# Kernel tuning notes

Measured on AMD Instinct MI355X. Metric: run time of the kernel, lower is better.

Reference implementation:

```python
import jax, jax.numpy as jnp
import numpy as np


def setup_inputs() -> dict:
    key = jax.random.key(0)
    ks = jax.random.split(key, 8)
    b, s1, s2 = 16, 512, 40
    video_dim, text_dim, attn_dim = 1024, 300, 256
    return {
        "video": jax.random.normal(ks[0], (b, s1, video_dim), dtype=jnp.float32),
        "text": jax.random.normal(ks[1], (b, s2, text_dim), dtype=jnp.float32),
        "w1": jax.random.normal(ks[2], (video_dim, attn_dim), dtype=jnp.float32),
        "w2": jax.random.normal(ks[3], (text_dim, attn_dim), dtype=jnp.float32),
        "w3": jax.random.normal(ks[4], (attn_dim, 1), dtype=jnp.float32),
        "bias": jax.random.normal(ks[5], (attn_dim,), dtype=jnp.float32),
        "w4": jax.random.normal(ks[6], (4 * attn_dim, 500), dtype=jnp.float32),
        "b4": jax.random.normal(ks[7], (500,), dtype=jnp.float32),
    }


def reference(video, text, w1, w2, w3, bias, w4, b4):
    # video: (b, s1, d1), text: (b, s2, d2)
    e = jnp.einsum("bsd,da->bsa", video, w1)   # (b, s1, a) -- also 'hh' in original
    f = jnp.einsum("btd,da->bta", text, w2)    # (b, s2, a)
    # additive attention energies: tanh over (b, s1, s2, a) broadcast sum
    h = jnp.tanh(e[:, :, None, :] + f[:, None, :, :] + bias)  # (b, s1, s2, a)
    logits = jnp.squeeze(jnp.einsum("bsta,ao->bsto", h, w3), -1)  # (b, s1, s2)
    # original expands logits over attn_dim then softmaxes dim=2; identical to
    # softmax over s2 of the scalar scores, broadcast afterwards.
    attn = jax.nn.softmax(logits, axis=2)  # (b, s1, s2)
    text_attn = jnp.einsum("bst,bta->bsa", attn, f)  # (b, s1, a)
    cont = jnp.concatenate(
        [e, text_attn, e * text_attn, e - text_attn], axis=-1
    )  # (b, s1, 4a)
    return jnp.tanh(cont) @ w4 + b4  # (b, s1, 500)
```

## Files before the change

kernel.cpp:

```cpp
#include <hip/hip_runtime.h>
#include <hip/hip_bf16.h>
#include <cstdint>

typedef __attribute__((ext_vector_type(8))) short bf16x8;
typedef __attribute__((ext_vector_type(4))) short bf16x4;
typedef __attribute__((ext_vector_type(4))) float f32x4;

#define TANH_SCALE 2.8853900817779268f
#define TANH_UNSCALE 0.34657359027997264f

__device__ __forceinline__ short cvt_bf16(float f) {
  union { float f; uint32_t u; } x; x.f = f;
  uint32_t r = x.u + 0x7FFFu + ((x.u >> 16) & 1u);
  return (short)(r >> 16);
}
__device__ __forceinline__ float bf16_to_f(short s) {
  union { uint32_t u; float f; } x; x.u = ((uint32_t)(uint16_t)s) << 16;
  return x.f;
}

__device__ __forceinline__ float tanh_fast(float x) {
  float e = __builtin_amdgcn_exp2f(x * TANH_SCALE);
  return 1.0f - 2.0f * __builtin_amdgcn_rcpf(e + 1.0f);
}
__device__ __forceinline__ float tanh_pre(float xs) {
  float e = __builtin_amdgcn_exp2f(xs);
  return 1.0f - 2.0f * __builtin_amdgcn_rcpf(e + 1.0f);
}

__global__ __launch_bounds__(256) void k_prep(const float* __restrict__ video,
                                              const float* __restrict__ text,
                                              const float* __restrict__ w1,
                                              const float* __restrict__ w2,
                                              const float* __restrict__ w4,
                                              short* __restrict__ vhi,
                                              short* __restrict__ vlo,
                                              short* __restrict__ w1h,
                                              short* __restrict__ w1l,
                                              short* __restrict__ w4T,
                                              short* __restrict__ th,
                                              short* __restrict__ tl,
                                              short* __restrict__ w2h,
                                              short* __restrict__ w2l) {
  __shared__ float tile[32][33];
  int bid = blockIdx.x;
  if (bid < 1024) {
    int i = bid * 256 + threadIdx.x;
    for (; i < 2097152; i += 1024 * 256) {
      float4 v = ((const float4*)video)[i];
      bf16x4 h, l;
      h.x = cvt_bf16(v.x); h.y = cvt_bf16(v.y); h.z = cvt_bf16(v.z); h.w = cvt_bf16(v.w);
      l.x = cvt_bf16(v.x - bf16_to_f(h.x));
      l.y = cvt_bf16(v.y - bf16_to_f(h.y));
      l.z = cvt_bf16(v.z - bf16_to_f(h.z));
      l.w = cvt_bf16(v.w - bf16_to_f(h.w));
      ((bf16x4*)vhi)[i] = h;
      ((bf16x4*)vlo)[i] = l;
    }
  } else if (bid < 1280) {
    int idx = bid - 1024;
    int r0 = (idx & 31) * 32, c0 = (idx >> 5) * 32;
    int j = threadIdx.x & 31, i0 = threadIdx.x >> 5;
    #pragma unroll
    for (int i = i0; i < 32; i += 8) tile[i][j] = w1[(size_t)(r0 + i) * 256 + c0 + j];
    __syncthreads();
    #pragma unroll
    for (int i = i0; i < 32; i += 8) {
      float v = tile[j][i];
      short h = cvt_bf16(v);
      w1h[(size_t)(c0 + i) * 1024 + r0 + j] = h;
      w1l[(size_t)(c0 + i) * 1024 + r0 + j] = cvt_bf16(v - bf16_to_f(h));
    }
  } else if (bid < 1792) {
    int idx = bid - 1280;
    int r0 = (idx & 31) * 32, c0 = (idx >> 5) * 32;
    int j = threadIdx.x & 31, i0 = threadIdx.x >> 5;
    #pragma unroll
    for (int i = i0; i < 32; i += 8) {
      int c = c0 + j;
      tile[i][j] = (c < 500) ? w4[(size_t)(r0 + i) * 500 + c] : 0.f;
    }
    __syncthreads();
    #pragma unroll
    for (int i = i0; i < 32; i += 8)
      w4T[(size_t)(c0 + i) * 1024 + r0 + j] = cvt_bf16(tile[j][i]);
  } else if (bid < 1952) {
    int idx = bid - 1792;
    int row = idx * 4 + (threadIdx.x >> 6);
    int cl = threadIdx.x & 63;
    const float* trow = text + (size_t)row * 300;
    short* hrow = th + (size_t)row * 320;
    short* lrow = tl + (size_t)row * 320;
    #pragma unroll
    for (int c0 = 0; c0 < 320; c0 += 64) {
      int c = c0 + cl;
      float v = (c < 300) ? trow[c] : 0.f;
      short h = cvt_bf16(v);
      hrow[c] = h;
      lrow[c] = cvt_bf16(v - bf16_to_f(h));
    }
  } else {
    int idx = bid - 1952;
    int rt = idx % 10, ct = idx / 10;
    int r0 = rt * 32, c0 = ct * 32;
    int j = threadIdx.x & 31, i0 = threadIdx.x >> 5;
    #pragma unroll
    for (int i = i0; i < 32; i += 8) {
      int r = r0 + i;
      tile[i][j] = (r < 300) ? w2[(size_t)r * 256 + c0 + j] : 0.f;
    }
    __syncthreads();
    #pragma unroll
    for (int i = i0; i < 32; i += 8) {
      float v = tile[j][i];
      short h = cvt_bf16(v);
      w2h[(size_t)(c0 + i) * 320 + r0 + j] = h;
      w2l[(size_t)(c0 + i) * 320 + r0 + j] = cvt_bf16(v - bf16_to_f(h));
    }
  }
}

__global__ __launch_bounds__(256) void k_gemm_split(const short* __restrict__ Ah,
                                                    const short* __restrict__ Al,
                                                    const short* __restrict__ BTh,
                                                    const short* __restrict__ BTl,
                                                    float* __restrict__ C,
                                                    int K, int ldc) {
  __shared__ __align__(16) short Ash[64][72];
  __shared__ __align__(16) short Asl[64][72];
  __shared__ __align__(16) short Bsh[64][72];
  __shared__ __align__(16) short Bsl[64][72];
  int m0 = blockIdx.x * 64, n0 = blockIdx.y * 64;
  int tid = threadIdx.x, lane = tid & 63, wave = tid >> 6;
  int wm = (wave & 1) * 32, wn = (wave >> 1) * 32;
  int srow = tid >> 3, sseg = (tid & 7) * 8;
  f32x4 acc[2][2];
  #pragma unroll
  for (int i = 0; i < 2; i++)
    #pragma unroll
    for (int j = 0; j < 2; j++) acc[i][j] = (f32x4){0.f, 0.f, 0.f, 0.f};
  int mrow = lane & 15, quad = lane >> 4;

  for (int k0 = 0; k0 < K; k0 += 64) {
    size_t aoff0 = (size_t)(m0 + srow) * K + k0 + sseg;
    size_t aoff1 = aoff0 + (size_t)32 * K;
    size_t boff0 = (size_t)(n0 + srow) * K + k0 + sseg;
    size_t boff1 = boff0 + (size_t)32 * K;
    bf16x8 a0h = *(const bf16x8*)(Ah + aoff0);
    bf16x8 a1h = *(const bf16x8*)(Ah + aoff1);
    bf16x8 a0l = *(const bf16x8*)(Al + aoff0);
    bf16x8 a1l = *(const bf16x8*)(Al + aoff1);
    bf16x8 b0h = *(const bf16x8*)(BTh + boff0);
    bf16x8 b1h = *(const bf16x8*)(BTh + boff1);
    bf16x8 b0l = *(const bf16x8*)(BTl + boff0);
    bf16x8 b1l = *(const bf16x8*)(BTl + boff1);
    __syncthreads();
    *(bf16x8*)&Ash[srow][sseg] = a0h;  *(bf16x8*)&Ash[srow + 32][sseg] = a1h;
    *(bf16x8*)&Asl[srow][sseg] = a0l;  *(bf16x8*)&Asl[srow + 32][sseg] = a1l;
    *(bf16x8*)&Bsh[srow][sseg] = b0h;  *(bf16x8*)&Bsh[srow + 32][sseg] = b1h;
    *(bf16x8*)&Bsl[srow][sseg] = b0l;  *(bf16x8*)&Bsl[srow + 32][sseg] = b1l;
    __syncthreads();
    #pragma unroll
    for (int ks = 0; ks < 2; ks++) {
      int kk = ks * 32 + quad * 8;
      bf16x8 ah[2], al[2], bh[2], bl[2];
      ah[0] = *(const bf16x8*)&Ash[wm + mrow][kk];
      ah[1] = *(const bf16x8*)&Ash[wm + 16 + mrow][kk];
      al[0] = *(const bf16x8*)&Asl[wm + mrow][kk];
      al[1] = *(const bf16x8*)&Asl[wm + 16 + mrow][kk];
      bh[0] = *(const bf16x8*)&Bsh[wn + mrow][kk];
      bh[1] = *(const bf16x8*)&Bsh[wn + 16 + mrow][kk];
      bl[0] = *(const bf16x8*)&Bsl[wn + mrow][kk];
      bl[1] = *(const bf16x8*)&Bsl[wn + 16 + mrow][kk];
      #pragma unroll
      for (int i = 0; i < 2; i++)
        #pragma unroll
        for (int j = 0; j < 2; j++) {
          acc[i][j] = __builtin_amdgcn_mfma_f32_16x16x32_bf16(ah[i], bh[j], acc[i][j], 0, 0, 0);
          acc[i][j] = __builtin_amdgcn_mfma_f32_16x16x32_bf16(ah[i], bl[j], acc[i][j], 0, 0, 0);
          acc[i][j] = __builtin_amdgcn_mfma_f32_16x16x32_bf16(al[i], bh[j], acc[i][j], 0, 0, 0);
        }
    }
  }
  int rbase = quad * 4;
  #pragma unroll
  for (int i = 0; i < 2; i++)
    #pragma unroll
    for (int j = 0; j < 2; j++) {
      int col = n0 + wn + j * 16 + mrow;
      #pragma unroll
      for (int r = 0; r < 4; r++) {
        int row = m0 + wm + i * 16 + rbase + r;
        C[(size_t)row * ldc + col] = acc[i][j][r];
      }
    }
}

__device__ __forceinline__ void load_lds16(void* lds, const void* g) {
  __builtin_amdgcn_global_load_lds(
      (const __attribute__((address_space(1))) void*)g,
      (__attribute__((address_space(3))) void*)lds, 16, 0, 0);
}

__global__ __launch_bounds__(256) void k_gemm_f(const short* __restrict__ A,
                                                const short* __restrict__ BT,
                                                const float* __restrict__ bias,
                                                float* __restrict__ C,
                                                int K, int ldc, int nstore) {
  __shared__ __align__(16) short As[128][64];
  __shared__ __align__(16) short Bs[64][64];
  int m0 = blockIdx.x * 128, n0 = blockIdx.y * 64;
  int tid = threadIdx.x, lane = tid & 63, wave = tid >> 6;
  int wm = wave * 32;
  int mrow = lane & 15, quad = lane >> 4;
  int lrow = lane >> 3, lseg = (lane & 7) * 8;

  f32x4 acc[2][4];
  #pragma unroll
  for (int i = 0; i < 2; i++)
    #pragma unroll
    for (int j = 0; j < 4; j++) acc[i][j] = (f32x4){0.f, 0.f, 0.f, 0.f};

  for (int k0 = 0; k0 < K; k0 += 64) {
    __syncthreads();
    #pragma unroll
    for (int i = 0; i < 4; i++) {
      int c = wave * 4 + i;
      load_lds16(&As[c * 8][0], A + (size_t)(m0 + c * 8 + lrow) * K + k0 + lseg);
    }
    #pragma unroll
    for (int i = 0; i < 2; i++) {
      int c = wave * 2 + i;
      load_lds16(&Bs[c * 8][0], BT + (size_t)(n0 + c * 8 + lrow) * K + k0 + lseg);
    }
    __syncthreads();
    #pragma unroll
    for (int ks = 0; ks < 2; ks++) {
      int kk = ks * 32 + quad * 8;
      bf16x8 af[2], bf[4];
      #pragma unroll
      for (int i = 0; i < 2; i++) af[i] = *(const bf16x8*)&As[wm + i * 16 + mrow][kk];
      #pragma unroll
      for (int j = 0; j < 4; j++) bf[j] = *(const bf16x8*)&Bs[j * 16 + mrow][kk];
      #pragma unroll
      for (int i = 0; i < 2; i++)
        #pragma unroll
        for (int j = 0; j < 4; j++)
          acc[i][j] = __builtin_amdgcn_mfma_f32_16x16x32_bf16(af[i], bf[j], acc[i][j], 0, 0, 0);
    }
  }
  int rbase = quad * 4;
  #pragma unroll
  for (int i = 0; i < 2; i++)
    #pragma unroll
    for (int j = 0; j < 4; j++) {
      int col = n0 + j * 16 + mrow;
      if (col < nstore) {
        float bv = bias[col];
        #pragma unroll
        for (int r = 0; r < 4; r++) {
          int row = m0 + wm + i * 16 + rbase + r;
          C[(size_t)row * ldc + col] = acc[i][j][r] + bv;
        }
      }
    }
}

__global__ __launch_bounds__(512) void k_middle(const float* __restrict__ e,
                                                const float* __restrict__ fb,
                                                const float* __restrict__ w3,
                                                const float* __restrict__ bias,
                                                short* __restrict__ cont) {
  __shared__ __align__(16) float fbs[40 * 256];
  __shared__ float lg[16][40];
  __shared__ float attn[16][40];
  int tid = threadIdx.x, wave = tid >> 6, lane = tid & 63;
  int la = lane & 31, half = lane >> 5;
  int row0 = blockIdx.x * 16;
  int b = row0 >> 9;
  int lgrow = wave + (half ? 8 : 0);
  int myrow = row0 + lgrow;

  const float4* fsrc = (const float4*)(fb + (size_t)b * 40 * 256);
  const float4* bias4 = (const float4*)bias;
  for (int i = tid; i < 40 * 64; i += 512) {
    float4 v = fsrc[i];
    float4 bb = bias4[i & 63];
    v.x = (v.x + bb.x) * TANH_SCALE; v.y = (v.y + bb.y) * TANH_SCALE;
    v.z = (v.z + bb.z) * TANH_SCALE; v.w = (v.w + bb.w) * TANH_SCALE;
    ((float4*)fbs)[i] = v;
  }
  __syncthreads();

  int a0 = la * 8;
  const float* erow = e + (size_t)myrow * 256 + a0;
  float4 e0 = *(const float4*)erow;
  float4 e1 = *(const float4*)(erow + 4);
  float4 w30 = *(const float4*)(w3 + a0);
  float4 w31 = *(const float4*)(w3 + a0 + 4);
  float4 bv0 = *(const float4*)(bias + a0);
  float4 bv1 = *(const float4*)(bias + a0 + 4);
  float4 es0, es1;
  es0.x = e0.x * TANH_SCALE; es0.y = e0.y * TANH_SCALE;
  es0.z = e0.z * TANH_SCALE; es0.w = e0.w * TANH_SCALE;
  es1.x = e1.x * TANH_SCALE; es1.y = e1.y * TANH_SCALE;
  es1.z = e1.z * TANH_SCALE; es1.w = e1.w * TANH_SCALE;

  for (int tc = 0; tc < 40; tc += 4) {
    float p[4];
    #pragma unroll
    for (int u = 0; u < 4; u++) {
      const float* fr = &fbs[(tc + u) * 256 + a0];
      float4 f0 = *(const float4*)fr;
      float4 f1 = *(const float4*)(fr + 4);
      p[u] = tanh_pre(es0.x + f0.x) * w30.x + tanh_pre(es0.y + f0.y) * w30.y
           + tanh_pre(es0.z + f0.z) * w30.z + tanh_pre(es0.w + f0.w) * w30.w
           + tanh_pre(es1.x + f1.x) * w31.x + tanh_pre(es1.y + f1.y) * w31.y
           + tanh_pre(es1.z + f1.z) * w31.z + tanh_pre(es1.w + f1.w) * w31.w;
    }
    #pragma unroll
    for (int s = 16; s >= 1; s >>= 1) {
      #pragma unroll
      for (int u = 0; u < 4; u++) p[u] += __shfl_xor(p[u], s, 64);
    }
    if (la == 0) {
      #pragma unroll
      for (int u = 0; u < 4; u++) lg[lgrow][tc + u] = p[u];
    }
  }

  auto softmax_row = [&](int r) {
    float x = (lane < 40) ? lg[r][lane] : -3.0e38f;
    float m = x;
    #pragma unroll
    for (int s = 32; s >= 1; s >>= 1) m = fmaxf(m, __shfl_xor(m, s, 64));
    float ex = (lane < 40) ? __builtin_amdgcn_exp2f((x - m) * 1.4426950408889634f) : 0.f;
    float ssum = ex;
    #pragma unroll
    for (int s = 32; s >= 1; s >>= 1) ssum += __shfl_xor(ssum, s, 64);
    if (lane < 40) attn[r][lane] = ex * __builtin_amdgcn_rcpf(ssum);
  };
  softmax_row(wave);
  softmax_row(wave + 8);

  float ac[8] = {0.f,0.f,0.f,0.f,0.f,0.f,0.f,0.f};
  for (int t = 0; t < 40; t++) {
    float w = attn[lgrow][t];
    const float* fr = &fbs[t * 256 + a0];
    float4 f0 = *(const float4*)fr;
    float4 f1 = *(const float4*)(fr + 4);
    ac[0] += w * f0.x; ac[1] += w * f0.y; ac[2] += w * f0.z; ac[3] += w * f0.w;
    ac[4] += w * f1.x; ac[5] += w * f1.y; ac[6] += w * f1.z; ac[7] += w * f1.w;
  }
  float tx[8];
  tx[0] = ac[0] * TANH_UNSCALE - bv0.x; tx[1] = ac[1] * TANH_UNSCALE - bv0.y;
  tx[2] = ac[2] * TANH_UNSCALE - bv0.z; tx[3] = ac[3] * TANH_UNSCALE - bv0.w;
  tx[4] = ac[4] * TANH_UNSCALE - bv1.x; tx[5] = ac[5] * TANH_UNSCALE - bv1.y;
  tx[6] = ac[6] * TANH_UNSCALE - bv1.z; tx[7] = ac[7] * TANH_UNSCALE - bv1.w;
  float ev[8] = {e0.x, e0.y, e0.z, e0.w, e1.x, e1.y, e1.z, e1.w};

  short* crow = cont + (size_t)myrow * 1024 + a0;
  auto st8 = [&](int off, const float* v) {
    bf16x8 pk;
    #pragma unroll
    for (int i = 0; i < 8; i++) pk[i] = cvt_bf16(v[i]);
    *(bf16x8*)(crow + off) = pk;
  };
  float s0[8], s1[8], s2[8], s3[8];
  #pragma unroll
  for (int i = 0; i < 8; i++) {
    s0[i] = tanh_fast(ev[i]);
    s1[i] = tanh_fast(tx[i]);
    s2[i] = tanh_fast(ev[i] * tx[i]);
    s3[i] = tanh_fast(ev[i] - tx[i]);
  }
  st8(0, s0); st8(256, s1); st8(512, s2); st8(768, s3);
}

extern "C" void kernel_launch(void* const* d_in, const int* in_sizes, int n_in,
                              void* d_out, int out_size, void* d_ws, size_t ws_size,
                              hipStream_t stream) {
  const float* video = (const float*)d_in[0];
  const float* text  = (const float*)d_in[1];
  const float* w1    = (const float*)d_in[2];
  const float* w2    = (const float*)d_in[3];
  const float* w3    = (const float*)d_in[4];
  const float* bias  = (const float*)d_in[5];
  const float* w4    = (const float*)d_in[6];
  const float* b4    = (const float*)d_in[7];
  float* out = (float*)d_out;
  char* ws = (char*)d_ws;

  short* video_hi = (short*)(ws);
  short* video_lo = (short*)(ws + 16777216);
  short* contbuf  = (short*)(ws + 16777216);
  short* w1T_hi   = (short*)(ws + 33554432);
  short* w1T_lo   = (short*)(ws + 34078720);
  short* w4T      = (short*)(ws + 34603008);
  float* fbuf     = (float*)(ws + 35651584);
  float* ebuf     = (float*)(ws + 36306944);
  short* text_hi  = (short*)(ws + 36306944);
  short* text_lo  = (short*)(ws + 36306944 + 409600);
  short* w2T_hi   = (short*)(ws + 36306944 + 819200);
  short* w2T_lo   = (short*)(ws + 36306944 + 1024000);

  k_prep<<<2032, 256, 0, stream>>>(video, text, w1, w2, w4,
                                   video_hi, video_lo, w1T_hi, w1T_lo, w4T,
                                   text_hi, text_lo, w2T_hi, w2T_lo);
  k_gemm_split<<<dim3(10, 4), 256, 0, stream>>>(text_hi, text_lo, w2T_hi, w2T_lo,
                                                fbuf, 320, 256);
  k_gemm_split<<<dim3(128, 4), 256, 0, stream>>>(video_hi, video_lo, w1T_hi, w1T_lo,
                                                 ebuf, 1024, 256);
  k_middle<<<512, 512, 0, stream>>>(ebuf, fbuf, w3, bias, contbuf);
  k_gemm_f<<<dim3(64, 8), 256, 0, stream>>>(contbuf, w4T, b4, out, 1024, 500, 500);
}
```

Measured before the change: 177.5 us.

## Split-K the video projection GEMM with larger M tiles, summing partials in middle kernel

```diff
diff --git a/kernel.cpp b/kernel.cpp
--- a/kernel.cpp
+++ b/kernel.cpp
@@ -202,6 +202,85 @@
       (__attribute__((address_space(3))) void*)lds, 16, 0, 0);
 }
 
+__global__ __launch_bounds__(256) void k_gemm_e2(const short* __restrict__ Ah,
+                                                 const short* __restrict__ Al,
+                                                 const short* __restrict__ BTh,
+                                                 const short* __restrict__ BTl,
+                                                 float* __restrict__ Cparts,
+                                                 int K, int ldc) {
+  __shared__ __align__(16) short Ash[128][64];
+  __shared__ __align__(16) short Asl[128][64];
+  __shared__ __align__(16) short Bsh[64][64];
+  __shared__ __align__(16) short Bsl[64][64];
+  int m0 = blockIdx.x * 128, n0 = blockIdx.y * 64;
+  int kz0 = blockIdx.z * 512;
+  int tid = threadIdx.x, lane = tid & 63, wave = tid >> 6;
+  int wm = wave * 32;
+  int mrow = lane & 15, quad = lane >> 4;
+  int lrow = lane >> 3, lseg = (lane & 7) * 8;
+
+  f32x4 acc[2][4];
+  #pragma unroll
+  for (int i = 0; i < 2; i++)
+    #pragma unroll
+    for (int j = 0; j < 4; j++) acc[i][j] = (f32x4){0.f, 0.f, 0.f, 0.f};
+
+  for (int k0 = kz0; k0 < kz0 + 512; k0 += 64) {
+    __syncthreads();
+    #pragma unroll
+    for (int i = 0; i < 4; i++) {
+      int c = wave * 4 + i;
+      size_t go = (size_t)(m0 + c * 8 + lrow) * K + k0 + lseg;
+      load_lds16(&Ash[c * 8][0], Ah + go);
+      load_lds16(&Asl[c * 8][0], Al + go);
+    }
+    #pragma unroll
+    for (int i = 0; i < 2; i++) {
+      int c = wave * 2 + i;
+      size_t go = (size_t)(n0 + c * 8 + lrow) * K + k0 + lseg;
+      load_lds16(&Bsh[c * 8][0], BTh + go);
+      load_lds16(&Bsl[c * 8][0], BTl + go);
+    }
+    __syncthreads();
+    #pragma unroll
+    for (int ks = 0; ks < 2; ks++) {
+      int kk = ks * 32 + quad * 8;
+      bf16x8 ah[2], al[2], bh[4], bl[4];
+      #pragma unroll
+      for (int i = 0; i < 2; i++) {
+        ah[i] = *(const bf16x8*)&Ash[wm + i * 16 + mrow][kk];
+        al[i] = *(const bf16x8*)&Asl[wm + i * 16 + mrow][kk];
+      }
+      #pragma unroll
+      for (int j = 0; j < 4; j++) {
+        bh[j] = *(const bf16x8*)&Bsh[j * 16 + mrow][kk];
+        bl[j] = *(const bf16x8*)&Bsl[j * 16 + mrow][kk];
+      }
+      #pragma unroll
+      for (int i = 0; i < 2; i++)
+        #pragma unroll
+        for (int j = 0; j < 4; j++) {
+          acc[i][j] = __builtin_amdgcn_mfma_f32_16x16x32_bf16(ah[i], bh[j], acc[i][j], 0, 0, 0);
+          acc[i][j] = __builtin_amdgcn_mfma_f32_16x16x32_bf16(ah[i], bl[j], acc[i][j], 0, 0, 0);
+          acc[i][j] = __builtin_amdgcn_mfma_f32_16x16x32_bf16(al[i], bh[j], acc[i][j], 0, 0, 0);
+        }
+    }
+  }
+  float* C = Cparts + (size_t)blockIdx.z * 8192 * 256;
+  int rbase = quad * 4;
+  #pragma unroll
+  for (int i = 0; i < 2; i++)
+    #pragma unroll
+    for (int j = 0; j < 4; j++) {
+      int col = n0 + j * 16 + mrow;
+      #pragma unroll
+      for (int r = 0; r < 4; r++) {
+        int row = m0 + wm + i * 16 + rbase + r;
+        C[(size_t)row * ldc + col] = acc[i][j][r];
+      }
+    }
+}
+
 __global__ __launch_bounds__(256) void k_gemm_f(const short* __restrict__ A,
                                                 const short* __restrict__ BT,
                                                 const float* __restrict__ bias,
@@ -266,7 +345,8 @@
     }
 }
 
-__global__ __launch_bounds__(512) void k_middle(const float* __restrict__ e,
+__global__ __launch_bounds__(512) void k_middle(const float* __restrict__ e0p,
+                                                const float* __restrict__ e1p,
                                                 const float* __restrict__ fb,
                                                 const float* __restrict__ w3,
                                                 const float* __restrict__ bias,
@@ -293,9 +373,14 @@
   __syncthreads();
 
   int a0 = la * 8;
-  const float* erow = e + (size_t)myrow * 256 + a0;
-  float4 e0 = *(const float4*)erow;
-  float4 e1 = *(const float4*)(erow + 4);
+  size_t eoff = (size_t)myrow * 256 + a0;
+  float4 p00 = *(const float4*)(e0p + eoff);
+  float4 p01 = *(const float4*)(e0p + eoff + 4);
+  float4 p10 = *(const float4*)(e1p + eoff);
+  float4 p11 = *(const float4*)(e1p + eoff + 4);
+  float4 e0, e1;
+  e0.x = p00.x + p10.x; e0.y = p00.y + p10.y; e0.z = p00.z + p10.z; e0.w = p00.w + p10.w;
+  e1.x = p01.x + p11.x; e1.y = p01.y + p11.y; e1.z = p01.z + p11.z; e1.w = p01.w + p11.w;
   float4 w30 = *(const float4*)(w3 + a0);
   float4 w31 = *(const float4*)(w3 + a0 + 4);
   float4 bv0 = *(const float4*)(bias + a0);
@@ -398,7 +483,8 @@
   short* w1T_lo   = (short*)(ws + 34078720);
   short* w4T      = (short*)(ws + 34603008);
   float* fbuf     = (float*)(ws + 35651584);
-  float* ebuf     = (float*)(ws + 36306944);
+  float* eparts   = (float*)(ws + 36306944);
+  float* epart1   = (float*)(ws + 36306944 + 8388608);
   short* text_hi  = (short*)(ws + 36306944);
   short* text_lo  = (short*)(ws + 36306944 + 409600);
   short* w2T_hi   = (short*)(ws + 36306944 + 819200);
@@ -409,8 +495,8 @@
                                    text_hi, text_lo, w2T_hi, w2T_lo);
   k_gemm_split<<<dim3(10, 4), 256, 0, stream>>>(text_hi, text_lo, w2T_hi, w2T_lo,
                                                 fbuf, 320, 256);
-  k_gemm_split<<<dim3(128, 4), 256, 0, stream>>>(video_hi, video_lo, w1T_hi, w1T_lo,
-                                                 ebuf, 1024, 256);
-  k_middle<<<512, 512, 0, stream>>>(ebuf, fbuf, w3, bias, contbuf);
+  k_gemm_e2<<<dim3(64, 4, 2), 256, 0, stream>>>(video_hi, video_lo, w1T_hi, w1T_lo,
+                                                eparts, 1024, 256);
+  k_middle<<<512, 512, 0, stream>>>(eparts, epart1, fbuf, w3, bias, contbuf);
   k_gemm_f<<<dim3(64, 8), 256, 0, stream>>>(contbuf, w4T, b4, out, 1024, 500, 500);
 }
```

Result: no change. 174.5 us (-1.7%).
